# Kernel tuning notes

Measured on AMD Instinct MI355X. Metric: run time of the kernel, lower is better.

Reference implementation:

```python
import jax, jax.numpy as jnp
import numpy as np
from jax import lax

GAMMA = 1.0  # RBFKernel gamma (init kwarg)


def setup_inputs() -> dict:
    key = jax.random.key(0)
    k1, k2, k3, k4, k5 = jax.random.split(key, 5)
    B, L, D = 2048, 128, 128  # L must equal D (inputs[i] reshaped to (1,1,D,D))
    return {
        "inputs": jax.random.normal(k1, (B, L, D), dtype=jnp.float32),
        "rotation_params": jax.random.normal(k2, (3 * D,), dtype=jnp.float32),
        "entangle_params": jax.random.normal(k3, (3 * D,), dtype=jnp.float32),
        "conv_w": jax.random.normal(k4, (1, 1, 2, 2), dtype=jnp.float32),
        "conv_b": jax.random.normal(k5, (1,), dtype=jnp.float32),
    }


def _conv_mean(inputs, conv_w, conv_b):
    # Vectorized version of the per-sample conv loop: (B, L, D) -> (B,)
    B, L, D = inputs.shape
    x = inputs.reshape(B, 1, D, D)
    y = lax.conv_general_dilated(
        x, conv_w, window_strides=(1, 1), padding="VALID",
        dimension_numbers=("NCHW", "OIHW", "NCHW"),
    ) + conv_b[None, :, None, None]
    return jnp.mean(y, axis=(1, 2, 3))  # (B,)


def reference(inputs, rotation_params, entangle_params, conv_w, conv_b):
    B, L, D = inputs.shape
    conv_out = _conv_mean(inputs, conv_w, conv_b)  # (B,), detached in torch via .item()

    rotation = rotation_params.reshape(D, -1)   # (D, 3)
    entangle = entangle_params.reshape(D, -1)   # (D, 3)
    query = inputs @ rotation                   # (B, L, 3)
    key_ = inputs @ entangle                    # (B, L, 3)

    # RBF kernel: exp(-gamma * ||q_i - k_j||^2) without materializing (B,L,L,3)
    q2 = jnp.sum(query * query, axis=-1)        # (B, L)
    k2 = jnp.sum(key_ * key_, axis=-1)          # (B, L)
    qk = jnp.einsum("bld,bmd->blm", query, key_)  # (B, L, L)
    dist2 = q2[:, :, None] + k2[:, None, :] - 2.0 * qk
    sim = jnp.exp(-GAMMA * dist2)               # (B, L, L)

    scores = jax.nn.softmax(sim, axis=-1)       # (B, L, L)
    attn_out = jnp.einsum("blm,bmd->bld", scores, inputs)  # (B, L, D)
    return attn_out + conv_out[:, None, None]
```

## Files before the change

kernel.cpp:

```cpp
#include <hip/hip_runtime.h>
#include <stdint.h>

typedef float f32x4 __attribute__((ext_vector_type(4)));
typedef float f32x2 __attribute__((ext_vector_type(2)));
typedef unsigned int u32x4 __attribute__((ext_vector_type(4)));

#define XP_OFF   0
#define RE_OFF   32768
#define QV_OFF   35840
#define KV_OFF   37888
#define WRED_OFF 39424
#define CORN_OFF 39552
#define CONV_OFF 39568
#define INV_OFF  39584
#define LDS_TOTAL 40096

__device__ __forceinline__ int rowswz(int row) {
  return ((row & 7) << 4) ^ (((row >> 3) & 1) << 6);
}
__device__ __forceinline__ f32x2 pk_fma(f32x2 a, f32x2 b, f32x2 c) {
  f32x2 d;
  asm("v_pk_fma_f32 %0, %1, %2, %3" : "=v"(d) : "v"(a), "v"(b), "v"(c));
  return d;
}
__device__ __forceinline__ f32x2 pk_add(f32x2 a, f32x2 b) {
  f32x2 d;
  asm("v_pk_add_f32 %0, %1, %2" : "=v"(d) : "v"(a), "v"(b));
  return d;
}
__device__ __forceinline__ f32x2 pk_mul(f32x2 a, f32x2 b) {
  f32x2 d;
  asm("v_pk_mul_f32 %0, %1, %2" : "=v"(d) : "v"(a), "v"(b));
  return d;
}
__device__ __forceinline__ uint32_t cvtpk(float lo, float hi) {
  uint32_t r;
  asm("v_cvt_pk_bf16_f32 %0, %1, %2" : "=v"(r) : "v"(lo), "v"(hi));
  return r;
}


__global__ __launch_bounds__(256, 4)
void hsa_fused(const float* __restrict__ xall,
               const float* __restrict__ rotp,
               const float* __restrict__ entp,
               const float* __restrict__ cw,
               const float* __restrict__ cb,
               float* __restrict__ out) {
  __shared__ __align__(16) char lds[LDS_TOTAL];
  float* wred  = (float*)(lds + WRED_OFF);
  float* corn  = (float*)(lds + CORN_OFF);
  float* convo = (float*)(lds + CONV_OFF);
  float* invar = (float*)(lds + INV_OFF);

  const int t   = threadIdx.x;
  const int wv  = t >> 6;
  const int l   = t & 63;
  const int lo  = l & 15;
  const int hi  = (l >> 4) & 3;
  const int r32 = l & 31;
  const int mh  = l >> 5;
  const int r   = t >> 1;
  const int h   = t & 1;
  const int b   = blockIdx.x;
  const float* xg = xall + (size_t)b * (128 * 128);

  f32x4 tl[16];
  {
    const f32x4* xrow4 = (const f32x4*)(xg + r * 128 + h * 64);
#pragma unroll
    for (int i = 0; i < 16; ++i) tl[i] = xrow4[i];
  }
  if (t < 128) {
    float* re = (float*)(lds + RE_OFF);
    re[t]        = rotp[3*t];   re[t + 128]  = rotp[3*t+1]; re[t + 256]  = rotp[3*t+2];
    re[t + 384]  = entp[3*t];   re[t + 512]  = entp[3*t+1]; re[t + 640]  = entp[3*t+2];
  }
  const f32x4 cwv = *(const f32x4*)cw;
  const float cbv = cb[0];
  {
    const int swr = rowswz(r);
    char* xrow = lds + XP_OFF + r * 256;
#pragma unroll
    for (int q = 0; q < 8; ++q) {
      u32x4 w;
      w[0] = cvtpk(tl[2*q][0],   tl[2*q][1]);
      w[1] = cvtpk(tl[2*q][2],   tl[2*q][3]);
      w[2] = cvtpk(tl[2*q+1][0], tl[2*q+1][1]);
      w[3] = cvtpk(tl[2*q+1][2], tl[2*q+1][3]);
      *(u32x4*)(xrow + ((h * 128 + q * 16) ^ swr)) = w;
    }
  }
  __syncthreads();

  f32x2 q0p={0.f,0.f}, q1p={0.f,0.f}, q2p={0.f,0.f};
  f32x2 k0p={0.f,0.f}, k1p={0.f,0.f}, k2p={0.f,0.f}, rsp={0.f,0.f};
  {
    const char* reb = lds + RE_OFF + h * 256;
#pragma unroll
    for (int s = 0; s < 16; ++s) {
      f32x4 r0 = *(const f32x4*)(reb + 0*512 + s*16);
      f32x4 r1 = *(const f32x4*)(reb + 1*512 + s*16);
      f32x4 r2 = *(const f32x4*)(reb + 2*512 + s*16);
      f32x4 e0 = *(const f32x4*)(reb + 3*512 + s*16);
      f32x4 e1 = *(const f32x4*)(reb + 4*512 + s*16);
      f32x4 e2 = *(const f32x4*)(reb + 5*512 + s*16);
      f32x4 xv = tl[s];
      f32x2 xlo = {xv[0], xv[1]}, xhi = {xv[2], xv[3]};
      q0p = pk_fma(xlo, (f32x2){r0[0],r0[1]}, q0p);
      q1p = pk_fma(xlo, (f32x2){r1[0],r1[1]}, q1p);
      q2p = pk_fma(xlo, (f32x2){r2[0],r2[1]}, q2p);
      k0p = pk_fma(xlo, (f32x2){e0[0],e0[1]}, k0p);
      k1p = pk_fma(xlo, (f32x2){e1[0],e1[1]}, k1p);
      k2p = pk_fma(xlo, (f32x2){e2[0],e2[1]}, k2p);
      rsp = pk_add(rsp, xlo);
      q0p = pk_fma(xhi, (f32x2){r0[2],r0[3]}, q0p);
      q1p = pk_fma(xhi, (f32x2){r1[2],r1[3]}, q1p);
      q2p = pk_fma(xhi, (f32x2){r2[2],r2[3]}, q2p);
      k0p = pk_fma(xhi, (f32x2){e0[2],e0[3]}, k0p);
      k1p = pk_fma(xhi, (f32x2){e1[2],e1[3]}, k1p);
      k2p = pk_fma(xhi, (f32x2){e2[2],e2[3]}, k2p);
      rsp = pk_add(rsp, xhi);
    }
  }
  float q0 = q0p[0]+q0p[1], q1 = q1p[0]+q1p[1], q2 = q2p[0]+q2p[1];
  float k0 = k0p[0]+k0p[1], k1 = k1p[0]+k1p[1], k2 = k2p[0]+k2p[1];
  float rs = rsp[0]+rsp[1];
  q0 += __shfl_xor(q0, 1); q1 += __shfl_xor(q1, 1); q2 += __shfl_xor(q2, 1);
  k0 += __shfl_xor(k0, 1); k1 += __shfl_xor(k1, 1); k2 += __shfl_xor(k2, 1);
  if (h == 0) {
    ((f32x4*)(lds + QV_OFF))[r] = (f32x4){q0, q1, q2, 0.f};
  } else {
    float* kv = (float*)(lds + KV_OFF);
    kv[r] = k0; kv[r + 128] = k1; kv[r + 256] = k2;
  }

  {
    float pA  = rs;
    float pR0 = (r == 0)   ? rs : 0.f;
    float pRL = (r == 127) ? rs : 0.f;
    float pC0 = (h == 0) ? tl[0][0]  : 0.f;
    float pCL = (h == 1) ? tl[15][3] : 0.f;
#pragma unroll
    for (int s = 32; s > 0; s >>= 1) {
      pA  += __shfl_xor(pA,  s);
      pR0 += __shfl_xor(pR0, s);
      pRL += __shfl_xor(pRL, s);
      pC0 += __shfl_xor(pC0, s);
      pCL += __shfl_xor(pCL, s);
    }
    if (l == 0) {
      wred[wv*8+0]=pA; wred[wv*8+1]=pR0; wred[wv*8+2]=pRL;
      wred[wv*8+3]=pC0; wred[wv*8+4]=pCL;
    }
    if (t == 0)   corn[0] = tl[0][0];
    if (t == 1)   corn[1] = tl[15][3];
    if (t == 254) corn[2] = tl[0][0];
    if (t == 255) corn[3] = tl[15][3];
  }

  u32x4 bfrag[2][4];
#pragma unroll
  for (int kt = 0; kt < 4; ++kt)
#pragma unroll
    for (int m = 0; m < 4; ++m) {
      const int k = kt * 32 + 8 * hi + 2 * m;
      const int rawb = wv * 64 + lo * 4;
      uint32_t A  = *(const uint32_t*)(lds + XP_OFF + k * 256 + (rawb ^ rowswz(k)));
      uint32_t Bv = *(const uint32_t*)(lds + XP_OFF + (k + 1) * 256 + (rawb ^ rowswz(k + 1)));
      bfrag[0][kt][m] = __builtin_amdgcn_perm(Bv, A, 0x05040100u);
      bfrag[1][kt][m] = __builtin_amdgcn_perm(Bv, A, 0x07060302u);
    }
  __syncthreads();

  if (t == 0) {
    float A  = wred[0]+wred[8]+wred[16]+wred[24];
    float R0 = wred[1]+wred[9]+wred[17]+wred[25];
    float RL = wred[2]+wred[10]+wred[18]+wred[26];
    float C0 = wred[3]+wred[11]+wred[19]+wred[27];
    float CL = wred[4]+wred[12]+wred[20]+wred[28];
    float S00 = A - RL - CL + corn[3];
    float S01 = A - RL - C0 + corn[2];
    float S10 = A - R0 - CL + corn[1];
    float S11 = A - R0 - C0 + corn[0];
    *convo = cbv + (cwv[0]*S00 + cwv[1]*S01 + cwv[2]*S10 + cwv[3]*S11) * (1.0f/16129.0f);
  }

  const int row = wv * 32 + r32;
  {
    f32x4 qrow = ((const f32x4*)(lds + QV_OFF))[row];
    f32x2 qq0 = {qrow[0], qrow[0]};
    f32x2 qq1 = {qrow[1], qrow[1]};
    f32x2 qq2 = {qrow[2], qrow[2]};
    const f32x2 m1   = {-1.f, -1.f};
    const f32x2 nl2e = {-1.4426950408889634f, -1.4426950408889634f};
    const f32x2 pl2e = { 1.4426950408889634f,  1.4426950408889634f};
    const char* kb = lds + KV_OFF;
    uint32_t wbuf[32];
    f32x2 denp = {0.f, 0.f};
#pragma unroll
    for (int i4 = 0; i4 < 16; ++i4) {
      const int m0 = mh * 64 + i4 * 4;
      f32x4 k0q = *(const f32x4*)(kb + 0    + m0 * 4);
      f32x4 k1q = *(const f32x4*)(kb + 512  + m0 * 4);
      f32x4 k2q = *(const f32x4*)(kb + 1024 + m0 * 4);
#pragma unroll
      for (int p = 0; p < 2; ++p) {
        f32x2 kp0 = {k0q[2*p], k0q[2*p+1]};
        f32x2 kp1 = {k1q[2*p], k1q[2*p+1]};
        f32x2 kp2 = {k2q[2*p], k2q[2*p+1]};
        f32x2 d0 = pk_fma(kp0, m1, qq0);
        f32x2 d1 = pk_fma(kp1, m1, qq1);
        f32x2 d2 = pk_fma(kp2, m1, qq2);
        f32x2 dist = pk_mul(d0, d0);
        dist = pk_fma(d1, d1, dist);
        dist = pk_fma(d2, d2, dist);
        f32x2 tt = pk_mul(dist, nl2e);
        f32x2 sim = {exp2f(tt[0]), exp2f(tt[1])};
        f32x2 uu = pk_mul(sim, pl2e);
        f32x2 ev = {exp2f(uu[0]), exp2f(uu[1])};
        denp = pk_add(denp, ev);
        wbuf[i4*2 + p] = cvtpk(ev[0], ev[1]);
      }
    }
    float den = denp[0] + denp[1];
    den += __shfl_xor(den, 32);
    float inv = 1.0f / den;
    if (mh == 0) invar[row] = inv;

    char* srow = lds + XP_OFF + row * 256;
    const int sw = rowswz(row);
#pragma unroll
    for (int u = 0; u < 8; ++u) {
      u32x4 w = { wbuf[u*4+0], wbuf[u*4+1], wbuf[u*4+2], wbuf[u*4+3] };
      *(u32x4*)(srow + ((mh * 128 + u * 16) ^ sw)) = w;
    }
  }
  __syncthreads();

  f32x4 acc[8][2];
#pragma unroll
  for (int mt = 0; mt < 8; ++mt)
#pragma unroll
    for (int n = 0; n < 2; ++n) acc[mt][n] = (f32x4){0.f,0.f,0.f,0.f};

#pragma unroll
  for (int mt = 0; mt < 8; ++mt) {
    const int arow = mt * 16 + lo;
    const char* ab = lds + XP_OFF + arow * 256;
    const int sw2 = rowswz(arow);
    u32x4 a0 = *(const u32x4*)(ab + ((0   + hi * 16) ^ sw2));
    u32x4 a1 = *(const u32x4*)(ab + ((64  + hi * 16) ^ sw2));
    u32x4 a2 = *(const u32x4*)(ab + ((128 + hi * 16) ^ sw2));
    u32x4 a3 = *(const u32x4*)(ab + ((192 + hi * 16) ^ sw2));
#pragma unroll
    for (int n = 0; n < 2; ++n) {
      asm volatile("v_mfma_f32_16x16x32_bf16 %0, %1, %2, %0"
                   : "+v"(acc[mt][n]) : "v"(a0), "v"(bfrag[n][0]));
      asm volatile("v_mfma_f32_16x16x32_bf16 %0, %1, %2, %0"
                   : "+v"(acc[mt][n]) : "v"(a1), "v"(bfrag[n][1]));
      asm volatile("v_mfma_f32_16x16x32_bf16 %0, %1, %2, %0"
                   : "+v"(acc[mt][n]) : "v"(a2), "v"(bfrag[n][2]));
      asm volatile("v_mfma_f32_16x16x32_bf16 %0, %1, %2, %0"
                   : "+v"(acc[mt][n]) : "v"(a3), "v"(bfrag[n][3]));
    }
  }
  asm volatile("s_nop 7\n\ts_nop 7"
               : "+v"(acc[0][0]), "+v"(acc[0][1]), "+v"(acc[1][0]), "+v"(acc[1][1]),
                 "+v"(acc[2][0]), "+v"(acc[2][1]), "+v"(acc[3][0]), "+v"(acc[3][1]),
                 "+v"(acc[4][0]), "+v"(acc[4][1]), "+v"(acc[5][0]), "+v"(acc[5][1]),
                 "+v"(acc[6][0]), "+v"(acc[6][1]), "+v"(acc[7][0]), "+v"(acc[7][1]));

  {
    float co = *convo;
    float* outb = out + (size_t)b * (128 * 128);
#pragma unroll
    for (int mt = 0; mt < 8; ++mt) {
      f32x4 invq = *(const f32x4*)(lds + INV_OFF + (mt * 16 + 4 * hi) * 4);
#pragma unroll
      for (int rr = 0; rr < 4; ++rr) {
        int rowg = mt * 16 + 4 * hi + rr;
        f32x2 v;
        v[0] = fmaf(acc[mt][0][rr], invq[rr], co);
        v[1] = fmaf(acc[mt][1][rr], invq[rr], co);
        __builtin_nontemporal_store(v, (f32x2*)(outb + rowg * 128 + wv * 32 + 2 * lo));
      }
    }
  }
}

extern "C" void kernel_launch(void* const* d_in, const int* in_sizes, int n_in,
                              void* d_out, int out_size, void* d_ws, size_t ws_size,
                              hipStream_t stream) {
  const float* x    = (const float*)d_in[0];
  const float* rotp = (const float*)d_in[1];
  const float* entp = (const float*)d_in[2];
  const float* cw   = (const float*)d_in[3];
  const float* cb   = (const float*)d_in[4];
  float* out = (float*)d_out;
  int B = in_sizes[0] >> 14;
  hipLaunchKernelGGL(hsa_fused, dim3(B), dim3(256), 0, stream,
                     x, rotp, entp, cw, cb, out);
}
```

Measured before the change: 53.48 us.

## Remap threads to two rows per quad-split with rotated LDS layout for Q/K

Each thread now handles two rows (r and r+64) split across four lanes per row instead of one row split across two lanes. The rotation/entangle parameters and key vectors get a rotated LDS layout (qrot) so the four lanes in a quad read different banks. The similarity stage reuses each loaded key quad for two query rows. The aim is fewer LDS bank conflicts and more reuse of LDS loads, at the cost of extra shuffle reductions and more live registers.

Measured after the change: 59.44 us. 11.1% more time.

```diff
diff --git a/kernel.cpp b/kernel.cpp
--- a/kernel.cpp
+++ b/kernel.cpp
@@ -17,6 +17,9 @@
 
 __device__ __forceinline__ int rowswz(int row) {
   return ((row & 7) << 4) ^ (((row >> 3) & 1) << 6);
+}
+__device__ __forceinline__ int qrot(int m) {
+  return ((m >> 5) << 7) + ((((m >> 2) + (m >> 5)) & 7) << 4) + ((m & 3) << 2);
 }
 __device__ __forceinline__ f32x2 pk_fma(f32x2 a, f32x2 b, f32x2 c) {
   f32x2 d;
@@ -58,89 +61,121 @@
   const int l   = t & 63;
   const int lo  = l & 15;
   const int hi  = (l >> 4) & 3;
-  const int r32 = l & 31;
-  const int mh  = l >> 5;
-  const int r   = t >> 1;
-  const int h   = t & 1;
+  const int rA  = t >> 2;
+  const int rB  = rA + 64;
+  const int qd  = t & 3;
   const int b   = blockIdx.x;
   const float* xg = xall + (size_t)b * (128 * 128);
 
   f32x4 tl[16];
   {
-    const f32x4* xrow4 = (const f32x4*)(xg + r * 128 + h * 64);
-#pragma unroll
-    for (int i = 0; i < 16; ++i) tl[i] = xrow4[i];
+    const f32x4* xa4 = (const f32x4*)(xg + rA * 128 + qd * 32);
+    const f32x4* xb4 = (const f32x4*)(xg + rB * 128 + qd * 32);
+#pragma unroll
+    for (int i = 0; i < 8; ++i) tl[i] = xa4[i];
+#pragma unroll
+    for (int i = 0; i < 8; ++i) tl[8 + i] = xb4[i];
   }
   if (t < 128) {
-    float* re = (float*)(lds + RE_OFF);
-    re[t]        = rotp[3*t];   re[t + 128]  = rotp[3*t+1]; re[t + 256]  = rotp[3*t+2];
-    re[t + 384]  = entp[3*t];   re[t + 512]  = entp[3*t+1]; re[t + 640]  = entp[3*t+2];
+    const int ro = qrot(t);
+    *(float*)(lds + RE_OFF + 0*512 + ro) = rotp[3*t];
+    *(float*)(lds + RE_OFF + 1*512 + ro) = rotp[3*t+1];
+    *(float*)(lds + RE_OFF + 2*512 + ro) = rotp[3*t+2];
+    *(float*)(lds + RE_OFF + 3*512 + ro) = entp[3*t];
+    *(float*)(lds + RE_OFF + 4*512 + ro) = entp[3*t+1];
+    *(float*)(lds + RE_OFF + 5*512 + ro) = entp[3*t+2];
   }
   const f32x4 cwv = *(const f32x4*)cw;
   const float cbv = cb[0];
   {
-    const int swr = rowswz(r);
-    char* xrow = lds + XP_OFF + r * 256;
-#pragma unroll
-    for (int q = 0; q < 8; ++q) {
-      u32x4 w;
-      w[0] = cvtpk(tl[2*q][0],   tl[2*q][1]);
-      w[1] = cvtpk(tl[2*q][2],   tl[2*q][3]);
-      w[2] = cvtpk(tl[2*q+1][0], tl[2*q+1][1]);
-      w[3] = cvtpk(tl[2*q+1][2], tl[2*q+1][3]);
-      *(u32x4*)(xrow + ((h * 128 + q * 16) ^ swr)) = w;
+    const int swA = rowswz(rA), swB = rowswz(rB);
+    char* rowa = lds + XP_OFF + rA * 256;
+    char* rowb = lds + XP_OFF + rB * 256;
+#pragma unroll
+    for (int j = 0; j < 4; ++j) {
+      u32x4 w, v;
+      w[0] = cvtpk(tl[2*j][0],   tl[2*j][1]);
+      w[1] = cvtpk(tl[2*j][2],   tl[2*j][3]);
+      w[2] = cvtpk(tl[2*j+1][0], tl[2*j+1][1]);
+      w[3] = cvtpk(tl[2*j+1][2], tl[2*j+1][3]);
+      v[0] = cvtpk(tl[8+2*j][0],   tl[8+2*j][1]);
+      v[1] = cvtpk(tl[8+2*j][2],   tl[8+2*j][3]);
+      v[2] = cvtpk(tl[8+2*j+1][0], tl[8+2*j+1][1]);
+      v[3] = cvtpk(tl[8+2*j+1][2], tl[8+2*j+1][3]);
+      *(u32x4*)(rowa + ((qd * 64 + j * 16) ^ swA)) = w;
+      *(u32x4*)(rowb + ((qd * 64 + j * 16) ^ swB)) = v;
     }
   }
   __syncthreads();
 
-  f32x2 q0p={0.f,0.f}, q1p={0.f,0.f}, q2p={0.f,0.f};
-  f32x2 k0p={0.f,0.f}, k1p={0.f,0.f}, k2p={0.f,0.f}, rsp={0.f,0.f};
-  {
-    const char* reb = lds + RE_OFF + h * 256;
-#pragma unroll
-    for (int s = 0; s < 16; ++s) {
-      f32x4 r0 = *(const f32x4*)(reb + 0*512 + s*16);
-      f32x4 r1 = *(const f32x4*)(reb + 1*512 + s*16);
-      f32x4 r2 = *(const f32x4*)(reb + 2*512 + s*16);
-      f32x4 e0 = *(const f32x4*)(reb + 3*512 + s*16);
-      f32x4 e1 = *(const f32x4*)(reb + 4*512 + s*16);
-      f32x4 e2 = *(const f32x4*)(reb + 5*512 + s*16);
-      f32x4 xv = tl[s];
-      f32x2 xlo = {xv[0], xv[1]}, xhi = {xv[2], xv[3]};
-      q0p = pk_fma(xlo, (f32x2){r0[0],r0[1]}, q0p);
-      q1p = pk_fma(xlo, (f32x2){r1[0],r1[1]}, q1p);
-      q2p = pk_fma(xlo, (f32x2){r2[0],r2[1]}, q2p);
-      k0p = pk_fma(xlo, (f32x2){e0[0],e0[1]}, k0p);
-      k1p = pk_fma(xlo, (f32x2){e1[0],e1[1]}, k1p);
-      k2p = pk_fma(xlo, (f32x2){e2[0],e2[1]}, k2p);
-      rsp = pk_add(rsp, xlo);
-      q0p = pk_fma(xhi, (f32x2){r0[2],r0[3]}, q0p);
-      q1p = pk_fma(xhi, (f32x2){r1[2],r1[3]}, q1p);
-      q2p = pk_fma(xhi, (f32x2){r2[2],r2[3]}, q2p);
-      k0p = pk_fma(xhi, (f32x2){e0[2],e0[3]}, k0p);
-      k1p = pk_fma(xhi, (f32x2){e1[2],e1[3]}, k1p);
-      k2p = pk_fma(xhi, (f32x2){e2[2],e2[3]}, k2p);
-      rsp = pk_add(rsp, xhi);
-    }
-  }
-  float q0 = q0p[0]+q0p[1], q1 = q1p[0]+q1p[1], q2 = q2p[0]+q2p[1];
-  float k0 = k0p[0]+k0p[1], k1 = k1p[0]+k1p[1], k2 = k2p[0]+k2p[1];
-  float rs = rsp[0]+rsp[1];
-  q0 += __shfl_xor(q0, 1); q1 += __shfl_xor(q1, 1); q2 += __shfl_xor(q2, 1);
-  k0 += __shfl_xor(k0, 1); k1 += __shfl_xor(k1, 1); k2 += __shfl_xor(k2, 1);
-  if (h == 0) {
-    ((f32x4*)(lds + QV_OFF))[r] = (f32x4){q0, q1, q2, 0.f};
-  } else {
-    float* kv = (float*)(lds + KV_OFF);
-    kv[r] = k0; kv[r + 128] = k1; kv[r + 256] = k2;
-  }
-
-  {
-    float pA  = rs;
-    float pR0 = (r == 0)   ? rs : 0.f;
-    float pRL = (r == 127) ? rs : 0.f;
-    float pC0 = (h == 0) ? tl[0][0]  : 0.f;
-    float pCL = (h == 1) ? tl[15][3] : 0.f;
+  f32x2 aq0={0.f,0.f}, aq1={0.f,0.f}, aq2={0.f,0.f};
+  f32x2 ak0={0.f,0.f}, ak1={0.f,0.f}, ak2={0.f,0.f};
+  f32x2 bq0={0.f,0.f}, bq1={0.f,0.f}, bq2={0.f,0.f};
+  f32x2 bk0={0.f,0.f}, bk1={0.f,0.f}, bk2={0.f,0.f};
+  f32x2 ars={0.f,0.f}, brs={0.f,0.f};
+  {
+    const char* reb = lds + RE_OFF + qd * 128;
+#pragma unroll
+    for (int s = 0; s < 8; ++s) {
+      const int rot = ((s + qd) & 7) << 4;
+      f32x4 r0 = *(const f32x4*)(reb + 0*512 + rot);
+      f32x4 r1 = *(const f32x4*)(reb + 1*512 + rot);
+      f32x4 r2 = *(const f32x4*)(reb + 2*512 + rot);
+      f32x4 e0 = *(const f32x4*)(reb + 3*512 + rot);
+      f32x4 e1 = *(const f32x4*)(reb + 4*512 + rot);
+      f32x4 e2 = *(const f32x4*)(reb + 5*512 + rot);
+      f32x4 xA = tl[s], xB = tl[8 + s];
+      f32x2 alo = {xA[0], xA[1]}, ahi = {xA[2], xA[3]};
+      f32x2 blo = {xB[0], xB[1]}, bhi = {xB[2], xB[3]};
+      f32x2 r0l = {r0[0],r0[1]}, r0h = {r0[2],r0[3]};
+      f32x2 r1l = {r1[0],r1[1]}, r1h = {r1[2],r1[3]};
+      f32x2 r2l = {r2[0],r2[1]}, r2h = {r2[2],r2[3]};
+      f32x2 e0l = {e0[0],e0[1]}, e0h = {e0[2],e0[3]};
+      f32x2 e1l = {e1[0],e1[1]}, e1h = {e1[2],e1[3]};
+      f32x2 e2l = {e2[0],e2[1]}, e2h = {e2[2],e2[3]};
+      aq0 = pk_fma(alo, r0l, aq0); aq0 = pk_fma(ahi, r0h, aq0);
+      aq1 = pk_fma(alo, r1l, aq1); aq1 = pk_fma(ahi, r1h, aq1);
+      aq2 = pk_fma(alo, r2l, aq2); aq2 = pk_fma(ahi, r2h, aq2);
+      ak0 = pk_fma(alo, e0l, ak0); ak0 = pk_fma(ahi, e0h, ak0);
+      ak1 = pk_fma(alo, e1l, ak1); ak1 = pk_fma(ahi, e1h, ak1);
+      ak2 = pk_fma(alo, e2l, ak2); ak2 = pk_fma(ahi, e2h, ak2);
+      ars = pk_add(ars, alo);      ars = pk_add(ars, ahi);
+      bq0 = pk_fma(blo, r0l, bq0); bq0 = pk_fma(bhi, r0h, bq0);
+      bq1 = pk_fma(blo, r1l, bq1); bq1 = pk_fma(bhi, r1h, bq1);
+      bq2 = pk_fma(blo, r2l, bq2); bq2 = pk_fma(bhi, r2h, bq2);
+      bk0 = pk_fma(blo, e0l, bk0); bk0 = pk_fma(bhi, e0h, bk0);
+      bk1 = pk_fma(blo, e1l, bk1); bk1 = pk_fma(bhi, e1h, bk1);
+      bk2 = pk_fma(blo, e2l, bk2); bk2 = pk_fma(bhi, e2h, bk2);
+      brs = pk_add(brs, blo);      brs = pk_add(brs, bhi);
+    }
+  }
+  float q0A = aq0[0]+aq0[1], q1A = aq1[0]+aq1[1], q2A = aq2[0]+aq2[1];
+  float k0A = ak0[0]+ak0[1], k1A = ak1[0]+ak1[1], k2A = ak2[0]+ak2[1];
+  float q0B = bq0[0]+bq0[1], q1B = bq1[0]+bq1[1], q2B = bq2[0]+bq2[1];
+  float k0B = bk0[0]+bk0[1], k1B = bk1[0]+bk1[1], k2B = bk2[0]+bk2[1];
+  float rsA = ars[0]+ars[1], rsB = brs[0]+brs[1];
+#define RED4(v) v += __shfl_xor(v, 1); v += __shfl_xor(v, 2);
+  RED4(q0A) RED4(q1A) RED4(q2A) RED4(k0A) RED4(k1A) RED4(k2A)
+  RED4(q0B) RED4(q1B) RED4(q2B) RED4(k0B) RED4(k1B) RED4(k2B)
+#undef RED4
+  if (qd == 0) {
+    ((f32x4*)(lds + QV_OFF))[rA] = (f32x4){q0A, q1A, q2A, 0.f};
+    ((f32x4*)(lds + QV_OFF))[rB] = (f32x4){q0B, q1B, q2B, 0.f};
+    const int oa = qrot(rA), ob = qrot(rB);
+    *(float*)(lds + KV_OFF + 0*512 + oa) = k0A;
+    *(float*)(lds + KV_OFF + 1*512 + oa) = k1A;
+    *(float*)(lds + KV_OFF + 2*512 + oa) = k2A;
+    *(float*)(lds + KV_OFF + 0*512 + ob) = k0B;
+    *(float*)(lds + KV_OFF + 1*512 + ob) = k1B;
+    *(float*)(lds + KV_OFF + 2*512 + ob) = k2B;
+  }
+
+  {
+    float pA  = rsA + rsB;
+    float pR0 = (rA == 0)  ? rsA : 0.f;
+    float pRL = (rA == 63) ? rsB : 0.f;
+    float pC0 = (qd == 0) ? (tl[0][0] + tl[8][0])  : 0.f;
+    float pCL = (qd == 3) ? (tl[7][3] + tl[15][3]) : 0.f;
 #pragma unroll
     for (int s = 32; s > 0; s >>= 1) {
       pA  += __shfl_xor(pA,  s);
@@ -154,8 +189,8 @@
       wred[wv*8+3]=pC0; wred[wv*8+4]=pCL;
     }
     if (t == 0)   corn[0] = tl[0][0];
-    if (t == 1)   corn[1] = tl[15][3];
-    if (t == 254) corn[2] = tl[0][0];
+    if (t == 3)   corn[1] = tl[7][3];
+    if (t == 252) corn[2] = tl[8][0];
     if (t == 255) corn[3] = tl[15][3];
   }
 
@@ -186,32 +221,31 @@
     *convo = cbv + (cwv[0]*S00 + cwv[1]*S01 + cwv[2]*S10 + cwv[3]*S11) * (1.0f/16129.0f);
   }
 
-  const int row = wv * 32 + r32;
-  {
-    f32x4 qrow = ((const f32x4*)(lds + QV_OFF))[row];
-    f32x2 qq0 = {qrow[0], qrow[0]};
-    f32x2 qq1 = {qrow[1], qrow[1]};
-    f32x2 qq2 = {qrow[2], qrow[2]};
+  {
+    f32x4 qav = ((const f32x4*)(lds + QV_OFF))[rA];
+    f32x4 qbv = ((const f32x4*)(lds + QV_OFF))[rB];
+    f32x2 qa0 = {qav[0], qav[0]}, qa1 = {qav[1], qav[1]}, qa2 = {qav[2], qav[2]};
+    f32x2 qb0 = {qbv[0], qbv[0]}, qb1 = {qbv[1], qbv[1]}, qb2 = {qbv[2], qbv[2]};
     const f32x2 m1   = {-1.f, -1.f};
     const f32x2 nl2e = {-1.4426950408889634f, -1.4426950408889634f};
     const f32x2 pl2e = { 1.4426950408889634f,  1.4426950408889634f};
-    const char* kb = lds + KV_OFF;
-    uint32_t wbuf[32];
-    f32x2 denp = {0.f, 0.f};
-#pragma unroll
-    for (int i4 = 0; i4 < 16; ++i4) {
-      const int m0 = mh * 64 + i4 * 4;
-      f32x4 k0q = *(const f32x4*)(kb + 0    + m0 * 4);
-      f32x4 k1q = *(const f32x4*)(kb + 512  + m0 * 4);
-      f32x4 k2q = *(const f32x4*)(kb + 1024 + m0 * 4);
+    const char* kb = lds + KV_OFF + qd * 128;
+    uint32_t wA[16], wB[16];
+    f32x2 dA = {0.f, 0.f}, dB = {0.f, 0.f};
+#pragma unroll
+    for (int i4 = 0; i4 < 8; ++i4) {
+      const int rot = ((i4 + qd) & 7) << 4;
+      f32x4 k0q = *(const f32x4*)(kb + 0*512 + rot);
+      f32x4 k1q = *(const f32x4*)(kb + 1*512 + rot);
+      f32x4 k2q = *(const f32x4*)(kb + 2*512 + rot);
 #pragma unroll
       for (int p = 0; p < 2; ++p) {
         f32x2 kp0 = {k0q[2*p], k0q[2*p+1]};
         f32x2 kp1 = {k1q[2*p], k1q[2*p+1]};
         f32x2 kp2 = {k2q[2*p], k2q[2*p+1]};
-        f32x2 d0 = pk_fma(kp0, m1, qq0);
-        f32x2 d1 = pk_fma(kp1, m1, qq1);
-        f32x2 d2 = pk_fma(kp2, m1, qq2);
+        f32x2 d0 = pk_fma(kp0, m1, qa0);
+        f32x2 d1 = pk_fma(kp1, m1, qa1);
+        f32x2 d2 = pk_fma(kp2, m1, qa2);
         f32x2 dist = pk_mul(d0, d0);
         dist = pk_fma(d1, d1, dist);
         dist = pk_fma(d2, d2, dist);
@@ -219,21 +253,39 @@
         f32x2 sim = {exp2f(tt[0]), exp2f(tt[1])};
         f32x2 uu = pk_mul(sim, pl2e);
         f32x2 ev = {exp2f(uu[0]), exp2f(uu[1])};
-        denp = pk_add(denp, ev);
-        wbuf[i4*2 + p] = cvtpk(ev[0], ev[1]);
+        dA = pk_add(dA, ev);
+        wA[i4*2 + p] = cvtpk(ev[0], ev[1]);
+        d0 = pk_fma(kp0, m1, qb0);
+        d1 = pk_fma(kp1, m1, qb1);
+        d2 = pk_fma(kp2, m1, qb2);
+        dist = pk_mul(d0, d0);
+        dist = pk_fma(d1, d1, dist);
+        dist = pk_fma(d2, d2, dist);
+        tt = pk_mul(dist, nl2e);
+        f32x2 sm2 = {exp2f(tt[0]), exp2f(tt[1])};
+        uu = pk_mul(sm2, pl2e);
+        f32x2 ev2 = {exp2f(uu[0]), exp2f(uu[1])};
+        dB = pk_add(dB, ev2);
+        wB[i4*2 + p] = cvtpk(ev2[0], ev2[1]);
       }
     }
-    float den = denp[0] + denp[1];
-    den += __shfl_xor(den, 32);
-    float inv = 1.0f / den;
-    if (mh == 0) invar[row] = inv;
-
-    char* srow = lds + XP_OFF + row * 256;
-    const int sw = rowswz(row);
-#pragma unroll
-    for (int u = 0; u < 8; ++u) {
-      u32x4 w = { wbuf[u*4+0], wbuf[u*4+1], wbuf[u*4+2], wbuf[u*4+3] };
-      *(u32x4*)(srow + ((mh * 128 + u * 16) ^ sw)) = w;
+    float denA = dA[0] + dA[1];
+    float denB = dB[0] + dB[1];
+    denA += __shfl_xor(denA, 1); denA += __shfl_xor(denA, 2);
+    denB += __shfl_xor(denB, 1); denB += __shfl_xor(denB, 2);
+    if (qd == 0) {
+      invar[rA] = 1.0f / denA;
+      invar[rB] = 1.0f / denB;
+    }
+    char* srA = lds + XP_OFF + rA * 256;
+    char* srB = lds + XP_OFF + rB * 256;
+    const int swA = rowswz(rA), swB = rowswz(rB);
+#pragma unroll
+    for (int j = 0; j < 4; ++j) {
+      u32x4 w = { wA[4*j+0], wA[4*j+1], wA[4*j+2], wA[4*j+3] };
+      u32x4 v = { wB[4*j+0], wB[4*j+1], wB[4*j+2], wB[4*j+3] };
+      *(u32x4*)(srA + ((qd * 64 + j * 16) ^ swA)) = w;
+      *(u32x4*)(srB + ((qd * 64 + j * 16) ^ swB)) = v;
     }
   }
   __syncthreads();
```
